# Kernel optimization log

Measured on AMD Instinct MI355X. Metric: run time of the kernel, lower is better.

## Reference

```python
import jax, jax.numpy as jnp
import numpy as np

T, B, I, H = 2048, 512, 1, 64


def setup_inputs() -> dict:
    key = jax.random.key(0)
    ks = jax.random.split(key, 8)
    s_in = 1.0 / np.sqrt(H)  # torch RNN/Linear init scale (uniform bound)
    return {
        "x": jax.random.normal(ks[0], (T, B, I), dtype=jnp.float32),
        "h": jax.random.normal(ks[1], (1, B, H), dtype=jnp.float32),
        "W_ih": jax.random.uniform(ks[2], (H, I), jnp.float32, -s_in, s_in),
        "W_hh": jax.random.uniform(ks[3], (H, H), jnp.float32, -s_in, s_in),
        "b_ih": jax.random.uniform(ks[4], (H,), jnp.float32, -s_in, s_in),
        "b_hh": jax.random.uniform(ks[5], (H,), jnp.float32, -s_in, s_in),
        "W_lin": jax.random.uniform(ks[6], (1, H), jnp.float32, -s_in, s_in),
        "b_lin": jax.random.uniform(ks[7], (1,), jnp.float32, -s_in, s_in),
    }


def reference(x, h, W_ih, W_hh, b_ih, b_hh, W_lin, b_lin):
    # tanh RNN: h_t = tanh(x_t W_ih^T + b_ih + h_{t-1} W_hh^T + b_hh)
    h0 = h[0]  # [B, H]
    # precompute input projection for all timesteps: [T, B, H]
    xp = jnp.einsum('tbi,hi->tbh', x, W_ih) + b_ih + b_hh

    def step(h_prev, xp_t):
        h_new = jnp.tanh(xp_t + h_prev @ W_hh.T)
        return h_new, h_new

    h_last, hs = jax.lax.scan(step, h0, xp)  # hs: [T, B, H]
    y = jnp.einsum('tbh,oh->tbo', hs, W_lin) + b_lin  # [T, B, 1]
    return y, h_last[None]  # h_n: [1, B, H]
```

## Files before the change

kernel.cpp:

```cpp
#include <hip/hip_runtime.h>

#define TT 2048
#define BB 512
#define HH 64
#define HIST 128
#define HPAD 68

typedef float f32x2 __attribute__((ext_vector_type(2)));
typedef float f32x4 __attribute__((ext_vector_type(4)));

#define FMA2(a, b, c) __builtin_elementwise_fma((a), (b), (c))
#define LO2(q) __builtin_shufflevector((q), (q), 0, 1)
#define HI2(q) __builtin_shufflevector((q), (q), 2, 3)

__global__ __launch_bounds__(64, 1) void rnn_fused(
    const float* __restrict__ x,
    const float* __restrict__ h0,
    const float* __restrict__ Wih,
    const float* __restrict__ Whh,
    const float* __restrict__ bih,
    const float* __restrict__ bhh,
    const float* __restrict__ Wlin,
    const float* __restrict__ blin,
    float* __restrict__ y,
    float* __restrict__ hN)
{
    __shared__ __align__(16) float hist[HIST][HPAD];
    __shared__ float xsh[TT + 4];
    __shared__ __align__(16) float wlin_sh[HH];

    const int b = blockIdx.x;
    const int h = threadIdx.x;

    for (int i = h; i < TT; i += 64)
        xsh[i] = x[(size_t)i * BB + b];
    if (h < 4) xsh[TT + h] = 0.f;

    f32x2 wr[32];
    const float* wp = Whh + h * HH;
#pragma unroll
    for (int i = 0; i < 32; ++i) {
        wr[i][0] = wp[2 * i + 0];
        wr[i][1] = wp[2 * i + 1];
    }
    const float wih  = Wih[h];
    const float bias = bih[h] + bhh[h];
    const float bl   = blin[0];

    wlin_sh[h] = Wlin[h];
    hist[HIST - 1][h] = h0[b * HH + h];

    float hval = 0.f;
    float xw = fmaf(xsh[0], wih, bias);

#pragma unroll 1
    for (int tc = 0; tc < TT; tc += HIST) {
#pragma unroll 4
        for (int ti = 0; ti < HIST; ++ti) {
            const int t  = tc + ti;
            const int rs = (ti + HIST - 1) & (HIST - 1);

            const f32x4* hp = reinterpret_cast<const f32x4*>(&hist[rs][0]);

            f32x2 a01 = {xw, 0.f}, a23 = {0.f, 0.f};
            f32x2 a45 = {0.f, 0.f}, a67 = {0.f, 0.f};
#pragma unroll
            for (int j = 0; j < 4; ++j) {
                const f32x4 p0 = hp[4 * j + 0];
                const f32x4 p1 = hp[4 * j + 1];
                const f32x4 p2 = hp[4 * j + 2];
                const f32x4 p3 = hp[4 * j + 3];
                a01 = FMA2(LO2(p0), wr[8 * j + 0], a01);
                a23 = FMA2(HI2(p0), wr[8 * j + 1], a23);
                a45 = FMA2(LO2(p1), wr[8 * j + 2], a45);
                a67 = FMA2(HI2(p1), wr[8 * j + 3], a67);
                a01 = FMA2(LO2(p2), wr[8 * j + 4], a01);
                a23 = FMA2(HI2(p2), wr[8 * j + 5], a23);
                a45 = FMA2(LO2(p3), wr[8 * j + 6], a45);
                a67 = FMA2(HI2(p3), wr[8 * j + 7], a67);
            }
            const f32x2 s2 = (a01 + a23) + (a45 + a67);
            const float acc = s2[0] + s2[1];

            const float e2 = __builtin_amdgcn_exp2f(acc * 2.885390081777927f);
            const float r  = __builtin_amdgcn_rcpf(e2 + 1.0f);
            hval = fmaf(-2.0f, r, 1.0f);

            hist[ti][h] = hval;

            xw = fmaf(xsh[t + 1], wih, bias);
        }

#pragma unroll 1
        for (int rep = 0; rep < 2; ++rep) {
            const int slot = rep * 64 + h;
            const f32x4* rp = reinterpret_cast<const f32x4*>(&hist[slot][0]);
            const f32x4* wl = reinterpret_cast<const f32x4*>(&wlin_sh[0]);
            f32x2 acc2 = {0.f, 0.f};
#pragma unroll
            for (int i = 0; i < 16; ++i) {
                const f32x4 q  = rp[i];
                const f32x4 qw = wl[i];
                acc2 = FMA2(LO2(q), LO2(qw), acc2);
                acc2 = FMA2(HI2(q), HI2(qw), acc2);
            }
            y[(size_t)(tc + slot) * BB + b] = acc2[0] + acc2[1] + bl;
        }
    }

    hN[b * HH + h] = hval;
}

extern "C" void kernel_launch(void* const* d_in, const int* in_sizes, int n_in,
                              void* d_out, int out_size, void* d_ws, size_t ws_size,
                              hipStream_t stream) {
    const float* x    = (const float*)d_in[0];
    const float* h0   = (const float*)d_in[1];
    const float* Wih  = (const float*)d_in[2];
    const float* Whh  = (const float*)d_in[3];
    const float* bih  = (const float*)d_in[4];
    const float* bhh  = (const float*)d_in[5];
    const float* Wlin = (const float*)d_in[6];
    const float* blin = (const float*)d_in[7];

    float* y  = (float*)d_out;
    float* hN = (float*)d_out + TT * BB;

    rnn_fused<<<dim3(BB), dim3(64), 0, stream>>>(x, h0, Wih, Whh, bih, bhh, Wlin, blin, y, hN);
}
```

Baseline: 347.1 us.

## Fetch own 16-lane row group via DPP instead of LDS in recurrence

Each thread's 16-element group of the previous hidden state is now gathered through DPP cross-lane moves in registers (with a permuted weight layout), so only 48 of the 64 hidden values are read from shared memory per step. The tanh scale constant is folded into the weights and bias to drop one multiply from the serial chain, and the history buffer is halved so the output projection runs in one pass per chunk. This cuts LDS read latency and bandwidth on the sequential critical path. In exchange it adds a chain of up to three dependent DPP ops and extra register use.

Result: slower. 464.5 us (+33.8%).

```diff
diff --git a/kernel.cpp b/kernel.cpp
--- a/kernel.cpp
+++ b/kernel.cpp
@@ -3,7 +3,7 @@
 #define TT 2048
 #define BB 512
 #define HH 64
-#define HIST 128
+#define HIST 64
 #define HPAD 68
 
 typedef float f32x2 __attribute__((ext_vector_type(2)));
@@ -12,6 +12,9 @@
 #define FMA2(a, b, c) __builtin_elementwise_fma((a), (b), (c))
 #define LO2(q) __builtin_shufflevector((q), (q), 0, 1)
 #define HI2(q) __builtin_shufflevector((q), (q), 2, 3)
+
+#define DPPM(v, ctrl) \
+    __int_as_float(__builtin_amdgcn_update_dpp(0, __float_as_int(v), (ctrl), 0xF, 0xF, false))
 
 __global__ __launch_bounds__(64, 1) void rnn_fused(
     const float* __restrict__ x,
@@ -25,90 +28,130 @@
     float* __restrict__ y,
     float* __restrict__ hN)
 {
+    __shared__ float wsh[HH * HH];
+    __shared__ float xsh[TT + 4];
     __shared__ __align__(16) float hist[HIST][HPAD];
-    __shared__ float xsh[TT + 4];
     __shared__ __align__(16) float wlin_sh[HH];
 
-    const int b = blockIdx.x;
-    const int h = threadIdx.x;
+    const int b  = blockIdx.x;
+    const int L  = threadIdx.x;
+    const int rb = L & 15;
+    const int R  = L >> 4;
 
-    for (int i = h; i < TT; i += 64)
-        xsh[i] = x[(size_t)i * BB + b];
-    if (h < 4) xsh[TT + h] = 0.f;
+    for (int i = L; i < HH * HH; i += 64) wsh[i] = Whh[i];
+    for (int i = L; i < TT; i += 64)      xsh[i] = x[(size_t)i * BB + b];
+    if (L < 4) xsh[TT + L] = 0.f;
+    wlin_sh[L] = Wlin[L];
 
-    f32x2 wr[32];
-    const float* wp = Whh + h * HH;
+    const float KSC = 2.885390081777927f;
+
+    float wd[16];
 #pragma unroll
-    for (int i = 0; i < 32; ++i) {
-        wr[i][0] = wp[2 * i + 0];
-        wr[i][1] = wp[2 * i + 1];
+    for (int m = 0; m < 16; ++m)
+        wd[m] = wsh[L * HH + 16 * R + (rb ^ m)] * KSC;
+
+    const int g1 = (R + 1) & 3, g2 = (R + 2) & 3, g3 = (R + 3) & 3;
+    f32x2 wA[8], wB[8], wC[8];
+#pragma unroll
+    for (int j = 0; j < 8; ++j) {
+        wA[j] = f32x2{wsh[L * HH + 16 * g1 + 2 * j], wsh[L * HH + 16 * g1 + 2 * j + 1]} * KSC;
+        wB[j] = f32x2{wsh[L * HH + 16 * g2 + 2 * j], wsh[L * HH + 16 * g2 + 2 * j + 1]} * KSC;
+        wC[j] = f32x2{wsh[L * HH + 16 * g3 + 2 * j], wsh[L * HH + 16 * g3 + 2 * j + 1]} * KSC;
     }
-    const float wih  = Wih[h];
-    const float bias = bih[h] + bhh[h];
-    const float bl   = blin[0];
+    const float wihs  = Wih[L] * KSC;
+    const float biass = (bih[L] + bhh[L]) * KSC;
+    const float bl    = blin[0];
+    const int off1 = 16 * g1, off2 = 16 * g2, off3 = 16 * g3;
 
-    wlin_sh[h] = Wlin[h];
-    hist[HIST - 1][h] = h0[b * HH + h];
-
-    float hval = 0.f;
-    float xw = fmaf(xsh[0], wih, bias);
+    hist[HIST - 1][L] = h0[(size_t)b * HH + L];
+    float hval = h0[(size_t)b * HH + L];
+    float xw   = fmaf(xsh[0], wihs, biass);
 
 #pragma unroll 1
     for (int tc = 0; tc < TT; tc += HIST) {
-#pragma unroll 4
+#pragma unroll 2
         for (int ti = 0; ti < HIST; ++ti) {
             const int t  = tc + ti;
             const int rs = (ti + HIST - 1) & (HIST - 1);
 
-            const f32x4* hp = reinterpret_cast<const f32x4*>(&hist[rs][0]);
+            const f32x4* ha = reinterpret_cast<const f32x4*>(&hist[rs][off1]);
+            const f32x4* hb = reinterpret_cast<const f32x4*>(&hist[rs][off2]);
+            const f32x4* hc = reinterpret_cast<const f32x4*>(&hist[rs][off3]);
+            const f32x4 A0 = ha[0], A1 = ha[1], A2 = ha[2], A3 = ha[3];
+            const f32x4 B0 = hb[0], B1 = hb[1], B2 = hb[2], B3 = hb[3];
+            const f32x4 C0 = hc[0], C1 = hc[1], C2 = hc[2], C3 = hc[3];
 
-            f32x2 a01 = {xw, 0.f}, a23 = {0.f, 0.f};
-            f32x2 a45 = {0.f, 0.f}, a67 = {0.f, 0.f};
-#pragma unroll
-            for (int j = 0; j < 4; ++j) {
-                const f32x4 p0 = hp[4 * j + 0];
-                const f32x4 p1 = hp[4 * j + 1];
-                const f32x4 p2 = hp[4 * j + 2];
-                const f32x4 p3 = hp[4 * j + 3];
-                a01 = FMA2(LO2(p0), wr[8 * j + 0], a01);
-                a23 = FMA2(HI2(p0), wr[8 * j + 1], a23);
-                a45 = FMA2(LO2(p1), wr[8 * j + 2], a45);
-                a67 = FMA2(HI2(p1), wr[8 * j + 3], a67);
-                a01 = FMA2(LO2(p2), wr[8 * j + 4], a01);
-                a23 = FMA2(HI2(p2), wr[8 * j + 5], a23);
-                a45 = FMA2(LO2(p3), wr[8 * j + 6], a45);
-                a67 = FMA2(HI2(p3), wr[8 * j + 7], a67);
-            }
-            const f32x2 s2 = (a01 + a23) + (a45 + a67);
-            const float acc = s2[0] + s2[1];
+            const float r0  = hval;
+            const float r1  = DPPM(hval, 0xB1);
+            const float r2  = DPPM(hval, 0x4E);
+            const float r3  = DPPM(r2,   0xB1);
+            const float r7  = DPPM(hval, 0x141);
+            const float r6  = DPPM(r7,   0xB1);
+            const float r5  = DPPM(r7,   0x4E);
+            const float r4  = DPPM(r5,   0xB1);
+            const float r15 = DPPM(hval, 0x140);
+            const float r14 = DPPM(r15,  0xB1);
+            const float r13 = DPPM(r15,  0x4E);
+            const float r12 = DPPM(r13,  0xB1);
+            const float r8  = DPPM(r15,  0x141);
+            const float r9  = DPPM(r8,   0xB1);
+            const float r10 = DPPM(r8,   0x4E);
+            const float r11 = DPPM(r10,  0xB1);
 
-            const float e2 = __builtin_amdgcn_exp2f(acc * 2.885390081777927f);
-            const float r  = __builtin_amdgcn_rcpf(e2 + 1.0f);
-            hval = fmaf(-2.0f, r, 1.0f);
+            float d0 = 0.f, d1 = 0.f, d2 = 0.f, d3 = 0.f;
+            d0 = fmaf(r0,  wd[0],  d0); d1 = fmaf(r1,  wd[1],  d1);
+            d2 = fmaf(r2,  wd[2],  d2); d3 = fmaf(r3,  wd[3],  d3);
+            d0 = fmaf(r4,  wd[4],  d0); d1 = fmaf(r5,  wd[5],  d1);
+            d2 = fmaf(r6,  wd[6],  d2); d3 = fmaf(r7,  wd[7],  d3);
+            d0 = fmaf(r8,  wd[8],  d0); d1 = fmaf(r9,  wd[9],  d1);
+            d2 = fmaf(r10, wd[10], d2); d3 = fmaf(r11, wd[11], d3);
+            d0 = fmaf(r12, wd[12], d0); d1 = fmaf(r13, wd[13], d1);
+            d2 = fmaf(r14, wd[14], d2); d3 = fmaf(r15, wd[15], d3);
 
-            hist[ti][h] = hval;
+            f32x2 aA = {xw, 0.f}, aA2 = {0.f, 0.f};
+            f32x2 aB = {0.f, 0.f}, aB2 = {0.f, 0.f};
+            f32x2 aC = {0.f, 0.f}, aC2 = {0.f, 0.f};
+            aA = FMA2(LO2(A0), wA[0], aA); aA2 = FMA2(HI2(A0), wA[1], aA2);
+            aA = FMA2(LO2(A1), wA[2], aA); aA2 = FMA2(HI2(A1), wA[3], aA2);
+            aA = FMA2(LO2(A2), wA[4], aA); aA2 = FMA2(HI2(A2), wA[5], aA2);
+            aA = FMA2(LO2(A3), wA[6], aA); aA2 = FMA2(HI2(A3), wA[7], aA2);
+            aB = FMA2(LO2(B0), wB[0], aB); aB2 = FMA2(HI2(B0), wB[1], aB2);
+            aB = FMA2(LO2(B1), wB[2], aB); aB2 = FMA2(HI2(B1), wB[3], aB2);
+            aB = FMA2(LO2(B2), wB[4], aB); aB2 = FMA2(HI2(B2), wB[5], aB2);
+            aB = FMA2(LO2(B3), wB[6], aB); aB2 = FMA2(HI2(B3), wB[7], aB2);
+            aC = FMA2(LO2(C0), wC[0], aC); aC2 = FMA2(HI2(C0), wC[1], aC2);
+            aC = FMA2(LO2(C1), wC[2], aC); aC2 = FMA2(HI2(C1), wC[3], aC2);
+            aC = FMA2(LO2(C2), wC[4], aC); aC2 = FMA2(HI2(C2), wC[5], aC2);
+            aC = FMA2(LO2(C3), wC[6], aC); aC2 = FMA2(HI2(C3), wC[7], aC2);
 
-            xw = fmaf(xsh[t + 1], wih, bias);
+            const f32x2 sv = ((aA + aA2) + (aB + aB2)) + (aC + aC2);
+            const float acc = (sv[0] + sv[1]) + ((d0 + d1) + (d2 + d3));
+
+            const float e2 = __builtin_amdgcn_exp2f(acc);
+            const float rc = __builtin_amdgcn_rcpf(e2 + 1.0f);
+            hval = fmaf(-2.0f, rc, 1.0f);
+
+            hist[ti][L] = hval;
+
+            xw = fmaf(xsh[t + 1], wihs, biass);
         }
 
-#pragma unroll 1
-        for (int rep = 0; rep < 2; ++rep) {
-            const int slot = rep * 64 + h;
-            const f32x4* rp = reinterpret_cast<const f32x4*>(&hist[slot][0]);
+        {
+            const f32x4* rp = reinterpret_cast<const f32x4*>(&hist[L][0]);
             const f32x4* wl = reinterpret_cast<const f32x4*>(&wlin_sh[0]);
-            f32x2 acc2 = {0.f, 0.f};
+            f32x2 a2 = {0.f, 0.f};
 #pragma unroll
             for (int i = 0; i < 16; ++i) {
                 const f32x4 q  = rp[i];
                 const f32x4 qw = wl[i];
-                acc2 = FMA2(LO2(q), LO2(qw), acc2);
-                acc2 = FMA2(HI2(q), HI2(qw), acc2);
+                a2 = FMA2(LO2(q), LO2(qw), a2);
+                a2 = FMA2(HI2(q), HI2(qw), a2);
             }
-            y[(size_t)(tc + slot) * BB + b] = acc2[0] + acc2[1] + bl;
+            y[(size_t)(tc + L) * BB + b] = a2[0] + a2[1] + bl;
         }
     }
 
-    hN[b * HH + h] = hval;
+    hN[(size_t)b * HH + L] = hval;
 }
 
 extern "C" void kernel_launch(void* const* d_in, const int* in_sizes, int n_in,
```
